# Performance work log

Hardware: AMD Instinct MI355X
Metric: run time of the kernel (lower is better)

## Reference

```python
import jax, jax.numpy as jnp
import numpy as np

N, E, C, H, W = 5000, 80000, 32, 8, 8


def setup_inputs() -> dict:
    key = jax.random.key(0)
    k1, k2, k3, k4, k5, k6 = jax.random.split(key, 6)
    h = jax.random.normal(k1, (N, C, H, W), dtype=jnp.float32)
    e = jax.random.uniform(k2, (E,), dtype=jnp.float32)
    src = jax.random.randint(k3, (E,), 0, N, dtype=jnp.int32)
    # ensure every node receives at least one message (avoids -inf segments),
    # matching a connected graph where update_all covers all nodes
    dst = jnp.concatenate([jnp.arange(N, dtype=jnp.int32),
                           jax.random.randint(k4, (E - N,), 0, N, dtype=jnp.int32)])
    fan_in = C * 3 * 3
    bound = float(1.0 / np.sqrt(fan_in))
    conv_w = jax.random.uniform(k5, (C, C, 3, 3), minval=-bound, maxval=bound, dtype=jnp.float32)
    conv_b = jax.random.uniform(k6, (C,), minval=-bound, maxval=bound, dtype=jnp.float32)
    return {"h": h, "e": e, "conv_w": conv_w, "conv_b": conv_b, "src": src, "dst": dst}


def reference(h, e, conv_w, conv_b, src, dst):
    # message: gather source features per edge, scale by scalar edge weight
    m = e[:, None, None, None] * h[src]                      # [E, C, H, W]
    # conv2d(dim->dim, k=3, pad=1) + exact GELU, edges as batch dim
    m = jax.lax.conv_general_dilated(
        m, conv_w, window_strides=(1, 1), padding='SAME',
        dimension_numbers=('NCHW', 'OIHW', 'NCHW'))
    m = jax.nn.gelu(m + conv_b[None, :, None, None], approximate=False)
    # reduce: ragged max over each destination node's mailbox
    out = jax.ops.segment_max(m, dst, num_segments=h.shape[0])  # [N, C, H, W]
    return out
```

## Files before the change

kernel.cpp:

```cpp
#include <hip/hip_runtime.h>
#include <math.h>

#define CCH   32
#define HWPIX 64
#define CHW   2048
#define HT_STRIDE 40
#define HT_NODE   2600

typedef __attribute__((ext_vector_type(8))) short bf16x8;
typedef __attribute__((ext_vector_type(4))) float f32x4;
typedef unsigned int uint_t;
typedef unsigned short ushort_t;

__device__ __forceinline__ ushort_t f2bf(float f) {
    uint_t u = __float_as_uint(f);
    u += 0x7fffu + ((u >> 16) & 1u);
    return (ushort_t)(u >> 16);
}

__device__ __forceinline__ float fgelu(float x) {
    float x2 = x * x;
    float t = x * fmaf(0.0713548162726f, x2, 1.5957691216f);
    float ez = __expf(-t);
    return x * __builtin_amdgcn_rcpf(1.0f + ez);
}


__global__ __launch_bounds__(256) void hist_prep_kernel(
    const int* __restrict__ dst, int* cnt, int ne, int nhist,
    const float* __restrict__ w, ushort_t* __restrict__ wfrag) {
    int b = blockIdx.x;
    if (b < nhist) {
        int i = b * 256 + threadIdx.x;
        if (i < ne) atomicAdd(&cnt[dst[i]], 1);
    } else {
        for (int idx = threadIdx.x; idx < 18 * 64; idx += 256) {
            int ch = idx / (9 * 64);
            int rem = idx % (9 * 64);
            int tap = rem / 64;
            int l = rem % 64;
            int co = ch * 16 + (l & 15);
            int g = l >> 4;
            for (int j = 0; j < 8; j++) {
                int ci = g * 8 + j;
                wfrag[(size_t)idx * 8 + j] = f2bf(w[(co * CCH + ci) * 9 + tap]);
            }
        }
    }
}

__global__ __launch_bounds__(256) void scan_kernel(const int* __restrict__ cnt,
                                                   int* __restrict__ offs,
                                                   int* __restrict__ cursor,
                                                   int nn) {
    __shared__ int part[256];
    int t = threadIdx.x;
    int per = (nn + 255) >> 8;
    if (per > 32) per = 32;
    int base = t * per;
    int local[32];
    int sum = 0;
    for (int i = 0; i < per; i++) {
        int idx = base + i;
        int v = (idx < nn) ? cnt[idx] : 0;
        local[i] = sum;
        sum += v;
    }
    part[t] = sum;
    __syncthreads();
    int acc = sum;
    for (int d = 1; d < 256; d <<= 1) {
        int tv = (t >= d) ? part[t - d] : 0;
        __syncthreads();
        acc += tv;
        part[t] = acc;
        __syncthreads();
    }
    int excl = acc - sum;
    for (int i = 0; i < per; i++) {
        int idx = base + i;
        if (idx < nn) {
            int o = excl + local[i];
            offs[idx] = o;
            cursor[idx] = o;
        }
    }
    if (t == 255) offs[nn] = acc;
}

__global__ __launch_bounds__(256) void conv_scatter_kernel(
    const float* __restrict__ h, const ushort_t* __restrict__ wfrag,
    ushort_t* __restrict__ convh, int nconv,
    const int* __restrict__ dst, const int* __restrict__ src,
    const float* __restrict__ e, int* cursor, int2* __restrict__ swA, int ne) {
    __shared__ ushort_t Ht[2 * HT_NODE];
    int b = blockIdx.x;
    int t = threadIdx.x;

    if (b >= nconv) {
        int i = (b - nconv) * 256 + t;
        if (i < ne) {
            int p = atomicAdd(&cursor[dst[i]], 1);
            int2 v;
            v.x = src[i];
            v.y = __float_as_int(e[i]);
            swA[p] = v;
        }
        return;
    }

    int node0 = b * 2;
    uint_t* Hd = (uint_t*)Ht;
#pragma unroll
    for (int nd = 0; nd < 2; nd++) {
        const float* hn = h + (size_t)(node0 + nd) * CHW;
#pragma unroll
        for (int it = 0; it < 4; it++) {
            int ci2 = it * 4 + (t >> 6);
            int p = t & 63;
            float a = hn[ci2 * 128 + p];
            float bb = hn[ci2 * 128 + 64 + p];
            uint_t val = (uint_t)f2bf(a) | ((uint_t)f2bf(bb) << 16);
            Hd[nd * (HT_NODE / 2) + p * (HT_STRIDE / 2) + ci2] = val;
        }
    }
    if (t < 40) Hd[0 * (HT_NODE / 2) + 64 * (HT_STRIDE / 2) + (t % 20)] = 0;
    if (t >= 40 && t < 80) Hd[1 * (HT_NODE / 2) + 64 * (HT_STRIDE / 2) + (t - 40) % 20] = 0;
    __syncthreads();

    int l = t & 63;
    int w = __builtin_amdgcn_readfirstlane(t >> 6);
    int nd = w >> 1;
    int ch = w & 1;
    int s = l & 15, g = l >> 4;
    int n = node0 + nd;

    bf16x8 A[9];
#pragma unroll
    for (int tap = 0; tap < 9; tap++)
        A[tap] = ((const bf16x8*)wfrag)[(ch * 9 + tap) * 64 + l];

    f32x4 C[4];
#pragma unroll
    for (int i = 0; i < 4; i++) C[i] = (f32x4){0.f, 0.f, 0.f, 0.f};

    const short* HtS = (const short*)(Ht + nd * HT_NODE);
#pragma unroll
    for (int tau = 0; tau < 4; tau++) {
        int p = tau * 16 + s;
        int y = p >> 3, x = p & 7;
#pragma unroll
        for (int tap = 0; tap < 9; tap++) {
            int dy = tap / 3 - 1, dx = tap % 3 - 1;
            int yy = y + dy, xx = x + dx;
            bool valid = (yy >= 0) & (yy < 8) & (xx >= 0) & (xx < 8);
            int pp = valid ? (yy * 8 + xx) : 64;
            bf16x8 B = *(const bf16x8*)&HtS[pp * HT_STRIDE + g * 8];
            C[tau] = __builtin_amdgcn_mfma_f32_16x16x32_bf16(A[tap], B, C[tau], 0, 0, 0);
        }
    }

    ushort_t* outn = convh + (size_t)n * CHW;
#pragma unroll
    for (int tau = 0; tau < 4; tau++) {
        uint_t lo = (uint_t)f2bf(C[tau][0]) | ((uint_t)f2bf(C[tau][1]) << 16);
        uint_t hi = (uint_t)f2bf(C[tau][2]) | ((uint_t)f2bf(C[tau][3]) << 16);
        uint2 v; v.x = lo; v.y = hi;
        *(uint2*)(outn + (tau * 16 + s) * 32 + ch * 16 + g * 4) = v;
    }
}

__device__ __forceinline__ void red8(float* mn, float* mx, uint4 q, float wg) {
    uint_t u0 = q.x, u1 = q.y, u2 = q.z, u3 = q.w;
    float v;
    v = wg * __uint_as_float(u0 << 16);          mn[0] = fminf(mn[0], v); mx[0] = fmaxf(mx[0], v);
    v = wg * __uint_as_float(u0 & 0xffff0000u);  mn[1] = fminf(mn[1], v); mx[1] = fmaxf(mx[1], v);
    v = wg * __uint_as_float(u1 << 16);          mn[2] = fminf(mn[2], v); mx[2] = fmaxf(mx[2], v);
    v = wg * __uint_as_float(u1 & 0xffff0000u);  mn[3] = fminf(mn[3], v); mx[3] = fmaxf(mx[3], v);
    v = wg * __uint_as_float(u2 << 16);          mn[4] = fminf(mn[4], v); mx[4] = fmaxf(mx[4], v);
    v = wg * __uint_as_float(u2 & 0xffff0000u);  mn[5] = fminf(mn[5], v); mx[5] = fmaxf(mx[5], v);
    v = wg * __uint_as_float(u3 << 16);          mn[6] = fminf(mn[6], v); mx[6] = fmaxf(mx[6], v);
    v = wg * __uint_as_float(u3 & 0xffff0000u);  mn[7] = fminf(mn[7], v); mx[7] = fmaxf(mx[7], v);
}

__global__ __launch_bounds__(256) void gather_max_kernel(
    const ushort_t* __restrict__ convh, const float* __restrict__ bias,
    const int* __restrict__ offs, const int2* __restrict__ swA,
    float* __restrict__ out) {
    int t = threadIdx.x;
    int l = t & 63;
    int w = t >> 6;
    int n = blockIdx.x * 2 + (w >> 1);
    int hf = w & 1;
    int beg = offs[n], end = offs[n + 1];
    int last = end - 1;

    const char* half_base = (const char*)convh + 2048 * hf + 16 * l;

    float mn[16], mx[16];
#pragma unroll
    for (int i = 0; i < 16; i++) { mn[i] = 3.402823466e+38f; mx[i] = -3.402823466e+38f; }

    int jB = (beg < last) ? beg + 1 : last;
    int2 sA = swA[beg], sB = swA[jB];
    const char* pA = half_base + (size_t)sA.x * 4096;
    const char* pB = half_base + (size_t)sB.x * 4096;
    uint4 A0 = *(const uint4*)pA, A1 = *(const uint4*)(pA + 1024);
    uint4 B0 = *(const uint4*)pB, B1 = *(const uint4*)(pB + 1024);
    float wgA = __int_as_float(sA.y), wgB = __int_as_float(sB.y);

    for (int j = beg; j < end; j += 2) {
        int jC = (j + 2 <= last) ? j + 2 : last;
        int jD = (j + 3 <= last) ? j + 3 : last;
        int2 sC = swA[jC];
        int2 sD = swA[jD];
        red8(mn, mx, A0, wgA);
        red8(mn + 8, mx + 8, A1, wgA);
        const char* pC = half_base + (size_t)sC.x * 4096;
        A0 = *(const uint4*)pC; A1 = *(const uint4*)(pC + 1024);
        wgA = __int_as_float(sC.y);
        red8(mn, mx, B0, wgB);
        red8(mn + 8, mx + 8, B1, wgB);
        const char* pD = half_base + (size_t)sD.x * 4096;
        B0 = *(const uint4*)pD; B1 = *(const uint4*)(pD + 1024);
        wgB = __int_as_float(sD.y);
    }

    const float4* b4 = (const float4*)(bias + (l & 3) * 8);
    float4 bLo = b4[0], bHi = b4[1];
    float bb[8] = {bLo.x, bLo.y, bLo.z, bLo.w, bHi.x, bHi.y, bHi.z, bHi.w};
    float* op = out + (size_t)n * CHW + (size_t)(l & 3) * 512 + hf * 32 + (l >> 2);
#pragma unroll
    for (int jj = 0; jj < 2; jj++) {
#pragma unroll
        for (int i = 0; i < 8; i++) {
            float xmx = mx[jj * 8 + i] + bb[i];
            float xmn = mn[jj * 8 + i] + bb[i];
            op[i * 64 + jj * 16] = fmaxf(fgelu(xmx), fgelu(xmn));
        }
    }
}

extern "C" void kernel_launch(void* const* d_in, const int* in_sizes, int n_in,
                              void* d_out, int out_size, void* d_ws, size_t ws_size,
                              hipStream_t stream) {
    const float* h      = (const float*)d_in[0];
    const float* e      = (const float*)d_in[1];
    const float* conv_w = (const float*)d_in[2];
    const float* conv_b = (const float*)d_in[3];
    const int*   src    = (const int*)d_in[4];
    const int*   dst    = (const int*)d_in[5];
    int nn = in_sizes[0] / CHW;
    int ne = in_sizes[1];

    ushort_t* convh = (ushort_t*)d_ws;
    ushort_t* wfrag = convh + (size_t)nn * CHW;
    int*   cnt    = (int*)(wfrag + 18 * 64 * 8);
    int*   offs   = cnt + nn;
    int*   cursor = offs + nn + 2;
    int2*  swA    = (int2*)(cursor + nn);

    int nhist = (ne + 255) / 256;
    int nconv = nn / 2;

    hipMemsetAsync(cnt, 0, (size_t)nn * sizeof(int), stream);
    hist_prep_kernel<<<nhist + 1, 256, 0, stream>>>(dst, cnt, ne, nhist,
                                                    conv_w, wfrag);
    scan_kernel<<<1, 256, 0, stream>>>(cnt, offs, cursor, nn);
    conv_scatter_kernel<<<nconv + nhist, 256, 0, stream>>>(
        h, wfrag, convh, nconv, dst, src, e, cursor, swA, ne);
    gather_max_kernel<<<nn / 2, 256, 0, stream>>>(convh, conv_b, offs, swA,
                                                  (float*)d_out);
}
```

Before: 169.5 us.

## Split gather-max work into quarter-node slices with deeper edge prefetch

The gather-max kernel now gives each wavefront one quarter (1 KB) of a node's conv row instead of a half. Each block covers four nodes for one quarter, and the grid doubles to nn blocks. The edge loop processes four edges per iteration and prefetches edge descriptors two groups ahead, so more loads are in flight per wave and fewer accumulator registers are needed. The cost is that edge index lists are read by twice as many waves, and neighbouring quarters of the same node land in different blocks, which may reduce L2 locality.

```diff
diff --git a/kernel.cpp b/kernel.cpp
--- a/kernel.cpp
+++ b/kernel.cpp
@@ -190,54 +190,58 @@
     int t = threadIdx.x;
     int l = t & 63;
     int w = t >> 6;
-    int n = blockIdx.x * 2 + (w >> 1);
-    int hf = w & 1;
+    int b = blockIdx.x;
+    int q = b & 3;
+    int n = (b >> 2) * 4 + w;
     int beg = offs[n], end = offs[n + 1];
     int last = end - 1;
 
-    const char* half_base = (const char*)convh + 2048 * hf + 16 * l;
-
-    float mn[16], mx[16];
-#pragma unroll
-    for (int i = 0; i < 16; i++) { mn[i] = 3.402823466e+38f; mx[i] = -3.402823466e+38f; }
-
-    int jB = (beg < last) ? beg + 1 : last;
-    int2 sA = swA[beg], sB = swA[jB];
-    const char* pA = half_base + (size_t)sA.x * 4096;
-    const char* pB = half_base + (size_t)sB.x * 4096;
-    uint4 A0 = *(const uint4*)pA, A1 = *(const uint4*)(pA + 1024);
-    uint4 B0 = *(const uint4*)pB, B1 = *(const uint4*)(pB + 1024);
-    float wgA = __int_as_float(sA.y), wgB = __int_as_float(sB.y);
-
-    for (int j = beg; j < end; j += 2) {
-        int jC = (j + 2 <= last) ? j + 2 : last;
-        int jD = (j + 3 <= last) ? j + 3 : last;
-        int2 sC = swA[jC];
-        int2 sD = swA[jD];
-        red8(mn, mx, A0, wgA);
-        red8(mn + 8, mx + 8, A1, wgA);
-        const char* pC = half_base + (size_t)sC.x * 4096;
-        A0 = *(const uint4*)pC; A1 = *(const uint4*)(pC + 1024);
-        wgA = __int_as_float(sC.y);
-        red8(mn, mx, B0, wgB);
-        red8(mn + 8, mx + 8, B1, wgB);
-        const char* pD = half_base + (size_t)sD.x * 4096;
-        B0 = *(const uint4*)pD; B1 = *(const uint4*)(pD + 1024);
-        wgB = __int_as_float(sD.y);
+    const char* qbase = (const char*)convh + 1024 * q + 16 * l;
+
+    float mn[8], mx[8];
+#pragma unroll
+    for (int i = 0; i < 8; i++) { mn[i] = 3.402823466e+38f; mx[i] = -3.402823466e+38f; }
+
+    int j1 = (beg + 1 < last) ? beg + 1 : last;
+    int j2 = (beg + 2 < last) ? beg + 2 : last;
+    int j3 = (beg + 3 < last) ? beg + 3 : last;
+    int2 d0 = swA[beg], d1 = swA[j1], d2 = swA[j2], d3 = swA[j3];
+    uint4 Q0 = *(const uint4*)(qbase + (size_t)d0.x * 4096);
+    uint4 Q1 = *(const uint4*)(qbase + (size_t)d1.x * 4096);
+    uint4 Q2 = *(const uint4*)(qbase + (size_t)d2.x * 4096);
+    uint4 Q3 = *(const uint4*)(qbase + (size_t)d3.x * 4096);
+    float W0 = __int_as_float(d0.y), W1 = __int_as_float(d1.y);
+    float W2 = __int_as_float(d2.y), W3 = __int_as_float(d3.y);
+    int k0 = (beg + 4 < last) ? beg + 4 : last;
+    int k1 = (beg + 5 < last) ? beg + 5 : last;
+    int k2 = (beg + 6 < last) ? beg + 6 : last;
+    int k3 = (beg + 7 < last) ? beg + 7 : last;
+    int2 S0 = swA[k0], S1 = swA[k1], S2 = swA[k2], S3 = swA[k3];
+
+    for (int j = beg; j < end; j += 4) {
+        int m0 = (j + 8 < last) ? j + 8 : last;
+        int m1 = (j + 9 < last) ? j + 9 : last;
+        int m2 = (j + 10 < last) ? j + 10 : last;
+        int m3 = (j + 11 < last) ? j + 11 : last;
+        int2 N0 = swA[m0], N1 = swA[m1], N2 = swA[m2], N3 = swA[m3];
+        red8(mn, mx, Q0, W0);
+        Q0 = *(const uint4*)(qbase + (size_t)S0.x * 4096); W0 = __int_as_float(S0.y);
+        red8(mn, mx, Q1, W1);
+        Q1 = *(const uint4*)(qbase + (size_t)S1.x * 4096); W1 = __int_as_float(S1.y);
+        red8(mn, mx, Q2, W2);
+        Q2 = *(const uint4*)(qbase + (size_t)S2.x * 4096); W2 = __int_as_float(S2.y);
+        red8(mn, mx, Q3, W3);
+        Q3 = *(const uint4*)(qbase + (size_t)S3.x * 4096); W3 = __int_as_float(S3.y);
+        S0 = N0; S1 = N1; S2 = N2; S3 = N3;
     }
 
     const float4* b4 = (const float4*)(bias + (l & 3) * 8);
     float4 bLo = b4[0], bHi = b4[1];
     float bb[8] = {bLo.x, bLo.y, bLo.z, bLo.w, bHi.x, bHi.y, bHi.z, bHi.w};
-    float* op = out + (size_t)n * CHW + (size_t)(l & 3) * 512 + hf * 32 + (l >> 2);
-#pragma unroll
-    for (int jj = 0; jj < 2; jj++) {
-#pragma unroll
-        for (int i = 0; i < 8; i++) {
-            float xmx = mx[jj * 8 + i] + bb[i];
-            float xmn = mn[jj * 8 + i] + bb[i];
-            op[i * 64 + jj * 16] = fmaxf(fgelu(xmx), fgelu(xmn));
-        }
+    float* op = out + (size_t)n * CHW + (size_t)(l & 3) * 512 + q * 16 + (l >> 2);
+#pragma unroll
+    for (int i = 0; i < 8; i++) {
+        op[i * 64] = fmaxf(fgelu(mx[i] + bb[i]), fgelu(mn[i] + bb[i]));
     }
 }
 
@@ -269,6 +273,6 @@
     scan_kernel<<<1, 256, 0, stream>>>(cnt, offs, cursor, nn);
     conv_scatter_kernel<<<nconv + nhist, 256, 0, stream>>>(
         h, wfrag, convh, nconv, dst, src, e, cursor, swA, ne);
-    gather_max_kernel<<<nn / 2, 256, 0, stream>>>(convh, conv_b, offs, swA,
-                                                  (float*)d_out);
-}
+    gather_max_kernel<<<nn, 256, 0, stream>>>(convh, conv_b, offs, swA,
+                                              (float*)d_out);
+}
```

New measurement: 153.7 us. 1.1x faster.
